# Kernel optimization log

Measured on AMD Instinct MI355X. Metric: run time of the kernel, lower is better.

Reference implementation:

```python
import jax, jax.numpy as jnp
import numpy as np

B, S, D, H = 2, 2048, 1024, 16
DK = D // H


def setup_inputs() -> dict:
    key = jax.random.key(0)
    ks = jax.random.split(key, 11)
    scale = 1.0 / np.sqrt(D)
    inp = {
        "k": jax.random.normal(ks[0], (B, S, D), jnp.float32),
        "q": jax.random.normal(ks[1], (B, S, D), jnp.float32),
        "v": jax.random.normal(ks[2], (B, S, D), jnp.float32),
        "w_q": jax.random.normal(ks[3], (D, D), jnp.float32) * scale,
        "b_q": jax.random.normal(ks[4], (D,), jnp.float32) * 0.01,
        "w_k": jax.random.normal(ks[5], (D, D), jnp.float32) * scale,
        "b_k": jax.random.normal(ks[6], (D,), jnp.float32) * 0.01,
        "w_v": jax.random.normal(ks[7], (D, D), jnp.float32) * scale,
        "b_v": jax.random.normal(ks[8], (D,), jnp.float32) * 0.01,
        "w_o": jax.random.normal(ks[9], (D, D), jnp.float32) * scale,
        "b_o": jax.random.normal(ks[10], (D,), jnp.float32) * 0.01,
        # causal mask; positions with mask==0 get -1e9 (masked_fill semantics)
        "mask": jnp.tril(jnp.ones((1, 1, S, S), jnp.int32)),
    }
    return inp


def reference(k, q, v, w_q, b_q, w_k, b_k, w_v, b_v, w_o, b_o, mask):
    MINUS_INF = -1000000000.0

    def proj(x, w, b):
        # nn.Linear: x @ w.T + b, then split heads -> [B, H, S, DK]
        y = x @ w.T + b
        return y.reshape(B, S, H, DK).transpose(0, 2, 1, 3)

    Q = proj(q, w_q, b_q)
    K = proj(k, w_k, b_k)
    V = proj(v, w_v, b_v)

    # [B, H, Sq, Sk] scores
    scores = jnp.einsum("bhqd,bhkd->bhqk", Q, K) / jnp.sqrt(jnp.float32(DK))
    scores = jnp.where(mask == 0, MINUS_INF, scores)
    attn = jax.nn.softmax(scores, axis=-1)

    out = jnp.einsum("bhqk,bhkd->bhqd", attn, V)  # [B, H, S, DK]
    out = out.transpose(0, 2, 1, 3).reshape(B, S, D)  # concat heads
    return out @ w_o.T + b_o
```

## Files before the change

kernel.cpp:

```cpp
#include <hip/hip_runtime.h>

typedef __bf16 bf16;
typedef __bf16 v8bf __attribute__((ext_vector_type(8)));
typedef __bf16 v4bf __attribute__((ext_vector_type(4)));
typedef float  v4f  __attribute__((ext_vector_type(4)));

#define MFMA16(a,b,c) __builtin_amdgcn_mfma_f32_16x16x32_bf16((a),(b),(c),0,0,0)

static constexpr int Sq = 2048;
static constexpr size_t NI = 4194304;
static constexpr size_t NW = 1048576;

__device__ __forceinline__ void gld_lds16(const void* g, void* l) {
  __builtin_amdgcn_global_load_lds(
      (__attribute__((address_space(1))) unsigned int*)g,
      (__attribute__((address_space(3))) unsigned int*)l,
      16, 0, 0);
}

__global__ __launch_bounds__(256) void convert_kernel(
    const float* __restrict__ q, const float* __restrict__ k, const float* __restrict__ v,
    const float* __restrict__ wq, const float* __restrict__ wk,
    const float* __restrict__ wv, const float* __restrict__ wo,
    bf16* __restrict__ dst)
{
  const int NI4 = 1048576;
  const int NW4 = 262144;
  int idx = blockIdx.x * 256 + threadIdx.x;
  const float* src; size_t dstoff; int local;
  if (idx < 3 * NI4) {
    int a = idx >> 20; local = idx & (NI4 - 1);
    src = (a == 0) ? q : ((a == 1) ? k : v);
    dstoff = (size_t)a * NI;
  } else {
    int t = idx - 3 * NI4;
    int a = t >> 18; local = t & (NW4 - 1);
    src = (a == 0) ? wq : ((a == 1) ? wk : ((a == 2) ? wv : wo));
    dstoff = 3 * NI + (size_t)a * NW;
  }
  float4 f = ((const float4*)src)[local];
  v4bf hv = { (bf16)f.x, (bf16)f.y, (bf16)f.z, (bf16)f.w };
  *(v4bf*)(dst + dstoff + (size_t)local * 4) = hv;
}

__device__ __forceinline__ void gemm_bt_body(
    const bf16* __restrict__ A, const bf16* __restrict__ Bw,
    const float* __restrict__ bias, bf16* __restrict__ outh,
    float* __restrict__ outf, int bm, int bn, int mode)
{
  __shared__ alignas(16) bf16 As[128 * 32];
  __shared__ alignas(16) bf16 Bs[128 * 32];
  const int tid = threadIdx.x;
  const int wave = tid >> 6, lane = tid & 63;
  const int quad = lane >> 4, l15 = lane & 15;
  const int wm = (wave >> 1) * 64, wn = (wave & 1) * 64;
  const int lrow = lane >> 2, lcol = (lane & 3) * 8;

  v4f acc[4][4];
#pragma unroll
  for (int i = 0; i < 4; i++)
#pragma unroll
    for (int j = 0; j < 4; j++) { v4f z = {0.f, 0.f, 0.f, 0.f}; acc[i][j] = z; }

  const bf16* gA = A  + (size_t)(bm + wave * 32 + lrow) * 1024 + lcol;
  const bf16* gB = Bw + (size_t)(bn + wave * 32 + lrow) * 1024 + lcol;
  bf16* lA0 = &As[(wave * 32) * 32];
  bf16* lA1 = &As[(wave * 32 + 16) * 32];
  bf16* lB0 = &Bs[(wave * 32) * 32];
  bf16* lB1 = &Bs[(wave * 32 + 16) * 32];

  for (int k0 = 0; k0 < 1024; k0 += 32) {
    gld_lds16(gA + k0, lA0);
    gld_lds16(gA + 16 * 1024 + k0, lA1);
    gld_lds16(gB + k0, lB0);
    gld_lds16(gB + 16 * 1024 + k0, lB1);
    __syncthreads();
    v8bf af[4], bfr[4];
#pragma unroll
    for (int i = 0; i < 4; i++)
      af[i] = *(const v8bf*)&As[(wm + i * 16 + l15) * 32 + quad * 8];
#pragma unroll
    for (int j = 0; j < 4; j++)
      bfr[j] = *(const v8bf*)&Bs[(wn + j * 16 + l15) * 32 + quad * 8];
#pragma unroll
    for (int i = 0; i < 4; i++)
#pragma unroll
      for (int j = 0; j < 4; j++)
        acc[i][j] = MFMA16(af[i], bfr[j], acc[i][j]);
    __syncthreads();
  }

#pragma unroll
  for (int i = 0; i < 4; i++) {
    const int m0 = bm + wm + i * 16 + quad * 4;
#pragma unroll
    for (int j = 0; j < 4; j++) {
      const int n = bn + wn + j * 16 + l15;
      const float bv = bias[n];
      if (mode == 1) {
#pragma unroll
        for (int r = 0; r < 4; r++)
          outf[(size_t)(m0 + r) * 1024 + n] = acc[i][j][r] + bv;
      } else if (mode == 2) {
        int b_ = m0 >> 11, s_ = m0 & 2047;
        int h_ = n >> 6,  dk = n & 63;
        v4bf pk;
#pragma unroll
        for (int r = 0; r < 4; r++) pk[r] = (bf16)(acc[i][j][r] + bv);
        *(v4bf*)&outh[((size_t)((b_ * 16 + h_) * 64 + dk)) * 2048 + s_] = pk;
      } else {
        const float sc = (mode == 3) ? 0.125f : 1.0f;
        int h_ = n >> 6,  dk = n & 63;
#pragma unroll
        for (int r = 0; r < 4; r++) {
          int m = m0 + r;
          int b_ = m >> 11, s_ = m & 2047;
          outh[(((size_t)(b_ * 16 + h_) * 2048 + s_) << 6) + dk] =
              (bf16)((acc[i][j][r] + bv) * sc);
        }
      }
    }
  }
}

__global__ __launch_bounds__(256, 2) void gemm_proj_kernel(
    const bf16* qb, const bf16* kb, const bf16* vb,
    const bf16* wqb, const bf16* wkb, const bf16* wvb,
    const float* bq, const float* bk, const float* bv,
    bf16* Qh, bf16* Kh, bf16* VhT)
{
  const bf16* A; const bf16* W; const float* bias; bf16* out; int mode;
  if (blockIdx.z == 0)      { A = qb; W = wqb; bias = bq; out = Qh;  mode = 3; }
  else if (blockIdx.z == 1) { A = kb; W = wkb; bias = bk; out = Kh;  mode = 0; }
  else                      { A = vb; W = wvb; bias = bv; out = VhT; mode = 2; }
  gemm_bt_body(A, W, bias, out, nullptr, blockIdx.y * 128, blockIdx.x * 128, mode);
}

__global__ __launch_bounds__(256, 2) void gemm_final_kernel(
    const bf16* Ob, const bf16* wob, const float* bo, float* out)
{
  gemm_bt_body(Ob, wob, bo, nullptr, out, blockIdx.y * 128, blockIdx.x * 128, 1);
}

__global__ __launch_bounds__(128, 2) void attn_kernel(
    const bf16* __restrict__ Qh, const bf16* __restrict__ Kh,
    const bf16* __restrict__ VhT, bf16* __restrict__ Ob)
{
  __shared__ alignas(16) bf16 Ps[2][32 * 72];
  const int tid = threadIdx.x;
  const int wave = tid >> 6, lane = tid & 63;
  const int quad = lane >> 4, l15 = lane & 15;
  const int bh = blockIdx.x, gy = blockIdx.y;
  const int b = bh >> 4, h = bh & 15;
  const int r8 = gy & 7, q8 = gy >> 3;
  const int u = 8 * q8 + ((q8 & 1) ? (7 - r8) : r8);
  const int qt = 2 * u + wave;
  const int L = u;
  const bf16* Qb = Qh + (size_t)bh * Sq * 64;
  const bf16* Kb = Kh + (size_t)bh * Sq * 64;
  const bf16* Vb = VhT + (size_t)bh * 64 * Sq;
  bf16* Pw = &Ps[wave][0];
  const int r0 = qt * 32;

  v8bf aq[2][2];
#pragma unroll
  for (int s = 0; s < 2; s++)
#pragma unroll
    for (int ks = 0; ks < 2; ks++)
      aq[s][ks] = *(const v8bf*)&Qb[(size_t)(r0 + s * 16 + l15) * 64 + ks * 32 + quad * 8];

  float lsum[2][4];
  v4f o[2][4];
#pragma unroll
  for (int s = 0; s < 2; s++)
#pragma unroll
    for (int r = 0; r < 4; r++) lsum[s][r] = 0.f;
#pragma unroll
  for (int s = 0; s < 2; s++)
#pragma unroll
    for (int j = 0; j < 4; j++) { v4f z = {0.f, 0.f, 0.f, 0.f}; o[s][j] = z; }

  auto loadK = [&](int kb, v8bf (&BK)[4][2]) {
#pragma unroll
    for (int n = 0; n < 4; n++) {
      BK[n][0] = *(const v8bf*)&Kb[(size_t)(kb + n * 16 + l15) * 64 + quad * 8];
      BK[n][1] = *(const v8bf*)&Kb[(size_t)(kb + n * 16 + l15) * 64 + 32 + quad * 8];
    }
  };
  auto loadV = [&](int kb, v8bf (&BV)[4][2]) {
#pragma unroll
    for (int n = 0; n < 4; n++) {
      BV[n][0] = *(const v8bf*)&Vb[(size_t)(n * 16 + l15) * 2048 + kb + quad * 8];
      BV[n][1] = *(const v8bf*)&Vb[(size_t)(n * 16 + l15) * 2048 + kb + 32 + quad * 8];
    }
  };
  auto compute = [&](const v8bf (&BK)[4][2], const v8bf (&BV)[4][2], int kc) {
    const int kbase = kc * 64;
    const bool diag = (kc == L);
#pragma unroll
    for (int s = 0; s < 2; s++) {
      v4f cn[4];
#pragma unroll
      for (int n = 0; n < 4; n++) {
        v4f z = {0.f, 0.f, 0.f, 0.f};
        cn[n] = MFMA16(aq[s][0], BK[n][0], z);
        cn[n] = MFMA16(aq[s][1], BK[n][1], cn[n]);
      }
      const int rbase = r0 + s * 16 + quad * 4;
#pragma unroll
      for (int n = 0; n < 4; n++) {
        const int colg = kbase + n * 16 + l15;
#pragma unroll
        for (int r = 0; r < 4; r++) {
          float e = __expf(cn[n][r]);
          if (diag && colg > rbase + r) e = 0.f;
          lsum[s][r] += e;
          Pw[(s * 16 + quad * 4 + r) * 72 + n * 16 + l15] = (bf16)e;
        }
      }
    }
#pragma unroll
    for (int s = 0; s < 2; s++) {
      v8bf ap0 = *(const v8bf*)&Pw[(s * 16 + l15) * 72 + quad * 8];
      v8bf ap1 = *(const v8bf*)&Pw[(s * 16 + l15) * 72 + 32 + quad * 8];
#pragma unroll
      for (int j = 0; j < 4; j++) {
        o[s][j] = MFMA16(ap0, BV[j][0], o[s][j]);
        o[s][j] = MFMA16(ap1, BV[j][1], o[s][j]);
      }
    }
  };

  v8bf bk0[4][2], bk1[4][2], bvv[4][2];
  loadK(0, bk0);
  int kc = 0;
  while (true) {
    loadV(kc * 64, bvv);
    if (kc < L) loadK((kc + 1) * 64, bk1);
    compute(bk0, bvv, kc);
    if (++kc > L) break;
    loadV(kc * 64, bvv);
    if (kc < L) loadK((kc + 1) * 64, bk0);
    compute(bk1, bvv, kc);
    if (++kc > L) break;
  }

#pragma unroll
  for (int s = 0; s < 2; s++)
#pragma unroll
    for (int r = 0; r < 4; r++) {
#pragma unroll
      for (int off = 1; off < 16; off <<= 1)
        lsum[s][r] += __shfl_xor(lsum[s][r], off, 64);
    }
#pragma unroll
  for (int s = 0; s < 2; s++)
#pragma unroll
    for (int r = 0; r < 4; r++) {
      const float inv = 1.0f / lsum[s][r];
      const int sg = r0 + s * 16 + quad * 4 + r;
#pragma unroll
      for (int j = 0; j < 4; j++)
        Ob[((size_t)(b * Sq + sg)) * 1024 + h * 64 + j * 16 + l15] =
            (bf16)(o[s][j][r] * inv);
    }
}

extern "C" void kernel_launch(void* const* d_in, const int* in_sizes, int n_in,
                              void* d_out, int out_size, void* d_ws, size_t ws_size,
                              hipStream_t stream) {
  (void)in_sizes; (void)n_in; (void)out_size; (void)ws_size;
  const float* kin = (const float*)d_in[0];
  const float* qin = (const float*)d_in[1];
  const float* vin = (const float*)d_in[2];
  const float* wq  = (const float*)d_in[3];
  const float* bq  = (const float*)d_in[4];
  const float* wk  = (const float*)d_in[5];
  const float* bk  = (const float*)d_in[6];
  const float* wv  = (const float*)d_in[7];
  const float* bv  = (const float*)d_in[8];
  const float* wo  = (const float*)d_in[9];
  const float* bo  = (const float*)d_in[10];

  bf16* ws = (bf16*)d_ws;
  bf16* qb  = ws;
  bf16* kb  = ws + NI;
  bf16* vb  = ws + 2 * NI;
  bf16* wqb = ws + 3 * NI;
  bf16* wkb = wqb + NW;
  bf16* wvb = wqb + 2 * NW;
  bf16* wob = wqb + 3 * NW;
  bf16* Qh  = ws + 3 * NI + 4 * NW;
  bf16* Kh  = Qh + NI;
  bf16* VhT = Qh + 2 * NI;
  bf16* Ob  = Qh + 3 * NI;

  convert_kernel<<<16384, 256, 0, stream>>>(qin, kin, vin, wq, wk, wv, wo, ws);
  gemm_proj_kernel<<<dim3(8, 32, 3), 256, 0, stream>>>(
      qb, kb, vb, wqb, wkb, wvb, bq, bk, bv, Qh, Kh, VhT);
  attn_kernel<<<dim3(32, 32), 128, 0, stream>>>(Qh, Kh, VhT, Ob);
  gemm_final_kernel<<<dim3(8, 32), 256, 0, stream>>>(Ob, wob, bo, (float*)d_out);
}
```

Measured before the change: 263.0 us.

## Split attention key loop across two waves per query tile and merge via LDS

Each block now owns a single 32-row query tile, and its two waves take alternating 64-key chunks instead of each wave owning a separate query tile. The partial outputs and row sums are exchanged through shared memory and combined before normalisation, and the grid is doubled. Occupancy hint rises to 4 blocks per CU. This is meant to balance causal work and expose more parallelism, at the cost of an extra LDS reduction, a block barrier, and more shared memory. The merge adds partial sums without rescaling, so it appears to rely on a fixed softmax offset rather than a per-wave running max.

New measurement: 405.5 us. +54.2%, slower.

```diff
diff --git a/kernel.cpp b/kernel.cpp
--- a/kernel.cpp
+++ b/kernel.cpp
@@ -142,20 +142,21 @@
   gemm_bt_body(Ob, wob, bo, nullptr, out, blockIdx.y * 128, blockIdx.x * 128, 1);
 }
 
-__global__ __launch_bounds__(128, 2) void attn_kernel(
+__global__ __launch_bounds__(128, 4) void attn_kernel(
     const bf16* __restrict__ Qh, const bf16* __restrict__ Kh,
     const bf16* __restrict__ VhT, bf16* __restrict__ Ob)
 {
   __shared__ alignas(16) bf16 Ps[2][32 * 72];
+  __shared__ alignas(16) float Xo[2][4][64][4];
+  __shared__ float Xl[2][64][4];
   const int tid = threadIdx.x;
   const int wave = tid >> 6, lane = tid & 63;
   const int quad = lane >> 4, l15 = lane & 15;
-  const int bh = blockIdx.x, gy = blockIdx.y;
+  const int bh = blockIdx.x, g = blockIdx.y;
   const int b = bh >> 4, h = bh & 15;
-  const int r8 = gy & 7, q8 = gy >> 3;
-  const int u = 8 * q8 + ((q8 & 1) ? (7 - r8) : r8);
-  const int qt = 2 * u + wave;
-  const int L = u;
+  const int a = g >> 3, rr = g & 7;
+  const int qt = 8 * a + ((a & 1) ? (7 - rr) : rr);
+  const int L = qt >> 1;
   const bf16* Qb = Qh + (size_t)bh * Sq * 64;
   const bf16* Kb = Kh + (size_t)bh * Sq * 64;
   const bf16* Vb = VhT + (size_t)bh * 64 * Sq;
@@ -232,38 +233,50 @@
   };
 
   v8bf bk0[4][2], bk1[4][2], bvv[4][2];
-  loadK(0, bk0);
-  int kc = 0;
-  while (true) {
-    loadV(kc * 64, bvv);
-    if (kc < L) loadK((kc + 1) * 64, bk1);
-    compute(bk0, bvv, kc);
-    if (++kc > L) break;
-    loadV(kc * 64, bvv);
-    if (kc < L) loadK((kc + 1) * 64, bk0);
-    compute(bk1, bvv, kc);
-    if (++kc > L) break;
-  }
-
-#pragma unroll
-  for (int s = 0; s < 2; s++)
-#pragma unroll
-    for (int r = 0; r < 4; r++) {
-#pragma unroll
-      for (int off = 1; off < 16; off <<= 1)
-        lsum[s][r] += __shfl_xor(lsum[s][r], off, 64);
-    }
-#pragma unroll
-  for (int s = 0; s < 2; s++)
-#pragma unroll
-    for (int r = 0; r < 4; r++) {
-      const float inv = 1.0f / lsum[s][r];
-      const int sg = r0 + s * 16 + quad * 4 + r;
-#pragma unroll
-      for (int j = 0; j < 4; j++)
-        Ob[((size_t)(b * Sq + sg)) * 1024 + h * 64 + j * 16 + l15] =
-            (bf16)(o[s][j][r] * inv);
-    }
+  int kc = wave;
+  if (kc <= L) {
+    loadK(kc * 64, bk0);
+    while (true) {
+      loadV(kc * 64, bvv);
+      if (kc + 2 <= L) loadK((kc + 2) * 64, bk1);
+      compute(bk0, bvv, kc);
+      kc += 2;
+      if (kc > L) break;
+      loadV(kc * 64, bvv);
+      if (kc + 2 <= L) loadK((kc + 2) * 64, bk0);
+      compute(bk1, bvv, kc);
+      kc += 2;
+      if (kc > L) break;
+    }
+  }
+
+  const int ow = 1 - wave;
+#pragma unroll
+  for (int j = 0; j < 4; j++)
+    *(v4f*)&Xo[wave][j][lane][0] = o[ow][j];
+#pragma unroll
+  for (int r = 0; r < 4; r++) Xl[wave][lane][r] = lsum[ow][r];
+  __syncthreads();
+
+  float ls[4];
+#pragma unroll
+  for (int r = 0; r < 4; r++) ls[r] = lsum[wave][r] + Xl[ow][lane][r];
+#pragma unroll
+  for (int off = 1; off < 16; off <<= 1)
+#pragma unroll
+    for (int r = 0; r < 4; r++) ls[r] += __shfl_xor(ls[r], off, 64);
+  v4f om[4];
+#pragma unroll
+  for (int j = 0; j < 4; j++) om[j] = o[wave][j] + *(const v4f*)&Xo[ow][j][lane][0];
+#pragma unroll
+  for (int r = 0; r < 4; r++) {
+    const float inv = 1.0f / ls[r];
+    const int sg = r0 + wave * 16 + quad * 4 + r;
+#pragma unroll
+    for (int j = 0; j < 4; j++)
+      Ob[((size_t)(b * Sq + sg)) * 1024 + h * 64 + j * 16 + l15] =
+          (bf16)(om[j][r] * inv);
+  }
 }
 
 extern "C" void kernel_launch(void* const* d_in, const int* in_sizes, int n_in,
@@ -298,6 +311,6 @@
   convert_kernel<<<16384, 256, 0, stream>>>(qin, kin, vin, wq, wk, wv, wo, ws);
   gemm_proj_kernel<<<dim3(8, 32, 3), 256, 0, stream>>>(
       qb, kb, vb, wqb, wkb, wvb, bq, bk, bv, Qh, Kh, VhT);
-  attn_kernel<<<dim3(32, 32), 128, 0, stream>>>(Qh, Kh, VhT, Ob);
+  attn_kernel<<<dim3(32, 64), 128, 0, stream>>>(Qh, Kh, VhT, Ob);
   gemm_final_kernel<<<dim3(8, 32), 256, 0, stream>>>(Ob, wob, bo, (float*)d_out);
 }
```

## Transpose attention MFMAs so each lane owns a query row, with swizzled LDS P

Applied to the files above, without the earlier changes.

Scores are now computed as K·Qᵀ, so each lane holds one query row. That lets the row sum reduce with two shuffles instead of four, lets P be written to LDS as packed 4-element vectors with an XOR swizzle and a halved buffer, and makes the output stores vectorised. The log2(e) factor is folded into the Q scaling so the kernel can use exp2f in place of __expf. The change trades a more complex indexing scheme for fewer LDS stores, fewer shuffles and fewer exp instructions, and correctness depends on getting the swizzle and transposed layouts right.

Measured after the change: 269.9 us. +2.6%, slower.

```diff
diff --git a/kernel.cpp b/kernel.cpp
--- a/kernel.cpp
+++ b/kernel.cpp
@@ -109,7 +109,7 @@
         for (int r = 0; r < 4; r++) pk[r] = (bf16)(acc[i][j][r] + bv);
         *(v4bf*)&outh[((size_t)((b_ * 16 + h_) * 64 + dk)) * 2048 + s_] = pk;
       } else {
-        const float sc = (mode == 3) ? 0.125f : 1.0f;
+        const float sc = (mode == 3) ? 0.18033688011112042f : 1.0f;
         int h_ = n >> 6,  dk = n & 63;
 #pragma unroll
         for (int r = 0; r < 4; r++) {
@@ -146,7 +146,7 @@
     const bf16* __restrict__ Qh, const bf16* __restrict__ Kh,
     const bf16* __restrict__ VhT, bf16* __restrict__ Ob)
 {
-  __shared__ alignas(16) bf16 Ps[2][32 * 72];
+  __shared__ alignas(16) bf16 Ps[2][16 * 72];
   const int tid = threadIdx.x;
   const int wave = tid >> 6, lane = tid & 63;
   const int quad = lane >> 4, l15 = lane & 15;
@@ -161,109 +161,107 @@
   const bf16* Vb = VhT + (size_t)bh * 64 * Sq;
   bf16* Pw = &Ps[wave][0];
   const int r0 = qt * 32;
-
-  v8bf aq[2][2];
-#pragma unroll
-  for (int s = 0; s < 2; s++)
+  const int xk = l15 & 7;
+
+  v8bf bq[2][2];
+#pragma unroll
+  for (int nt = 0; nt < 2; nt++)
 #pragma unroll
     for (int ks = 0; ks < 2; ks++)
-      aq[s][ks] = *(const v8bf*)&Qb[(size_t)(r0 + s * 16 + l15) * 64 + ks * 32 + quad * 8];
-
-  float lsum[2][4];
+      bq[nt][ks] = *(const v8bf*)&Qb[(size_t)(r0 + nt * 16 + l15) * 64 + ks * 32 + quad * 8];
+
+  float lsum[2] = {0.f, 0.f};
   v4f o[2][4];
 #pragma unroll
-  for (int s = 0; s < 2; s++)
-#pragma unroll
-    for (int r = 0; r < 4; r++) lsum[s][r] = 0.f;
-#pragma unroll
-  for (int s = 0; s < 2; s++)
-#pragma unroll
-    for (int j = 0; j < 4; j++) { v4f z = {0.f, 0.f, 0.f, 0.f}; o[s][j] = z; }
-
-  auto loadK = [&](int kb, v8bf (&BK)[4][2]) {
-#pragma unroll
-    for (int n = 0; n < 4; n++) {
-      BK[n][0] = *(const v8bf*)&Kb[(size_t)(kb + n * 16 + l15) * 64 + quad * 8];
-      BK[n][1] = *(const v8bf*)&Kb[(size_t)(kb + n * 16 + l15) * 64 + 32 + quad * 8];
+  for (int nt = 0; nt < 2; nt++)
+#pragma unroll
+    for (int j = 0; j < 4; j++) { v4f z = {0.f, 0.f, 0.f, 0.f}; o[nt][j] = z; }
+
+  auto loadK = [&](int kb, v8bf (&AK)[4][2]) {
+#pragma unroll
+    for (int m = 0; m < 4; m++) {
+      AK[m][0] = *(const v8bf*)&Kb[(size_t)(kb + m * 16 + l15) * 64 + quad * 8];
+      AK[m][1] = *(const v8bf*)&Kb[(size_t)(kb + m * 16 + l15) * 64 + 32 + quad * 8];
     }
   };
-  auto loadV = [&](int kb, v8bf (&BV)[4][2]) {
-#pragma unroll
-    for (int n = 0; n < 4; n++) {
-      BV[n][0] = *(const v8bf*)&Vb[(size_t)(n * 16 + l15) * 2048 + kb + quad * 8];
-      BV[n][1] = *(const v8bf*)&Vb[(size_t)(n * 16 + l15) * 2048 + kb + 32 + quad * 8];
+  auto loadV = [&](int kb, v8bf (&AV)[4][2]) {
+#pragma unroll
+    for (int j = 0; j < 4; j++) {
+      AV[j][0] = *(const v8bf*)&Vb[(size_t)(j * 16 + l15) * 2048 + kb + quad * 8];
+      AV[j][1] = *(const v8bf*)&Vb[(size_t)(j * 16 + l15) * 2048 + kb + 32 + quad * 8];
     }
   };
-  auto compute = [&](const v8bf (&BK)[4][2], const v8bf (&BV)[4][2], int kc) {
+  auto compute = [&](const v8bf (&AK)[4][2], const v8bf (&AV)[4][2], int kc) {
     const int kbase = kc * 64;
     const bool diag = (kc == L);
 #pragma unroll
-    for (int s = 0; s < 2; s++) {
+    for (int nt = 0; nt < 2; nt++) {
       v4f cn[4];
 #pragma unroll
-      for (int n = 0; n < 4; n++) {
+      for (int m = 0; m < 4; m++) {
         v4f z = {0.f, 0.f, 0.f, 0.f};
-        cn[n] = MFMA16(aq[s][0], BK[n][0], z);
-        cn[n] = MFMA16(aq[s][1], BK[n][1], cn[n]);
+        cn[m] = MFMA16(AK[m][0], bq[nt][0], z);
+        cn[m] = MFMA16(AK[m][1], bq[nt][1], cn[m]);
       }
-      const int rbase = r0 + s * 16 + quad * 4;
-#pragma unroll
-      for (int n = 0; n < 4; n++) {
-        const int colg = kbase + n * 16 + l15;
+      const int qrow = r0 + nt * 16 + l15;
+      const int rb = l15;
+#pragma unroll
+      for (int m = 0; m < 4; m++) {
+        const int keyb = kbase + m * 16 + quad * 4;
+        v4bf pk;
 #pragma unroll
         for (int r = 0; r < 4; r++) {
-          float e = __expf(cn[n][r]);
-          if (diag && colg > rbase + r) e = 0.f;
-          lsum[s][r] += e;
-          Pw[(s * 16 + quad * 4 + r) * 72 + n * 16 + l15] = (bf16)e;
+          float e = exp2f(cn[m][r]);
+          if (diag && (keyb + r > qrow)) e = 0.f;
+          lsum[nt] += e;
+          pk[r] = (bf16)e;
         }
+        const int ch = (2 * m + (quad >> 1)) ^ xk;
+        *(v4bf*)&Pw[rb * 72 + ch * 8 + (quad & 1) * 4] = pk;
       }
-    }
-#pragma unroll
-    for (int s = 0; s < 2; s++) {
-      v8bf ap0 = *(const v8bf*)&Pw[(s * 16 + l15) * 72 + quad * 8];
-      v8bf ap1 = *(const v8bf*)&Pw[(s * 16 + l15) * 72 + 32 + quad * 8];
-#pragma unroll
-      for (int j = 0; j < 4; j++) {
-        o[s][j] = MFMA16(ap0, BV[j][0], o[s][j]);
-        o[s][j] = MFMA16(ap1, BV[j][1], o[s][j]);
+#pragma unroll
+      for (int ks = 0; ks < 2; ks++) {
+        const int ch = (4 * ks + quad) ^ xk;
+        v8bf bp = *(const v8bf*)&Pw[rb * 72 + ch * 8];
+#pragma unroll
+        for (int j = 0; j < 4; j++)
+          o[nt][j] = MFMA16(AV[j][ks], bp, o[nt][j]);
       }
     }
   };
 
-  v8bf bk0[4][2], bk1[4][2], bvv[4][2];
-  loadK(0, bk0);
+  v8bf ak0[4][2], ak1[4][2], avv[4][2];
+  loadK(0, ak0);
   int kc = 0;
   while (true) {
-    loadV(kc * 64, bvv);
-    if (kc < L) loadK((kc + 1) * 64, bk1);
-    compute(bk0, bvv, kc);
+    loadV(kc * 64, avv);
+    if (kc < L) loadK((kc + 1) * 64, ak1);
+    compute(ak0, avv, kc);
     if (++kc > L) break;
-    loadV(kc * 64, bvv);
-    if (kc < L) loadK((kc + 1) * 64, bk0);
-    compute(bk1, bvv, kc);
+    loadV(kc * 64, avv);
+    if (kc < L) loadK((kc + 1) * 64, ak0);
+    compute(ak1, avv, kc);
     if (++kc > L) break;
   }
 
 #pragma unroll
-  for (int s = 0; s < 2; s++)
-#pragma unroll
-    for (int r = 0; r < 4; r++) {
-#pragma unroll
-      for (int off = 1; off < 16; off <<= 1)
-        lsum[s][r] += __shfl_xor(lsum[s][r], off, 64);
-    }
-#pragma unroll
-  for (int s = 0; s < 2; s++)
-#pragma unroll
-    for (int r = 0; r < 4; r++) {
-      const float inv = 1.0f / lsum[s][r];
-      const int sg = r0 + s * 16 + quad * 4 + r;
-#pragma unroll
-      for (int j = 0; j < 4; j++)
-        Ob[((size_t)(b * Sq + sg)) * 1024 + h * 64 + j * 16 + l15] =
-            (bf16)(o[s][j][r] * inv);
-    }
+  for (int nt = 0; nt < 2; nt++) {
+    lsum[nt] += __shfl_xor(lsum[nt], 16, 64);
+    lsum[nt] += __shfl_xor(lsum[nt], 32, 64);
+  }
+#pragma unroll
+  for (int nt = 0; nt < 2; nt++) {
+    const float inv = 1.0f / lsum[nt];
+    const int qrow = r0 + nt * 16 + l15;
+    bf16* dst = Ob + ((size_t)(b * Sq + qrow)) * 1024 + h * 64 + quad * 4;
+#pragma unroll
+    for (int j = 0; j < 4; j++) {
+      v4bf pk;
+#pragma unroll
+      for (int r = 0; r < 4; r++) pk[r] = (bf16)(o[nt][j][r] * inv);
+      *(v4bf*)(dst + j * 16) = pk;
+    }
+  }
 }
 
 extern "C" void kernel_launch(void* const* d_in, const int* in_sizes, int n_in,
```
